# Kernel optimization log

Hardware: AMD Instinct MI355X
Metric: run time of the kernel (lower is better)

The kernel has to match this reference:

```python
import jax, jax.numpy as jnp
import numpy as np
from jax import lax

S = 0.5      # smoothing coefficient (constant in the layer)
EPS = 1e-6   # numerical floor (constant in the layer)


def setup_inputs() -> dict:
    key = jax.random.key(0)
    # [1, F, T] nonnegative spectrogram-like input
    data = jax.random.uniform(key, (1, 1024, 16384), dtype=jnp.float32)
    alpha = jnp.float32(0.98)
    r = jnp.float32(0.5)
    delta = jnp.float32(2.0)
    return {"data": data, "alpha": alpha, "r": r, "delta": delta}


def _ema_over_time(x):
    # x: [F, T]; first-order IIR: m_t = (1-s)*m_{t-1} + s*x_t, m_{-1} = 0
    def step(carry, xt):  # carry, xt: [F]
        m = (1.0 - S) * carry + S * xt
        return m, m
    _, M = lax.scan(step, jnp.zeros(x.shape[0], x.dtype), x.T)  # M: [T, F]
    return M.T  # [F, T]


def reference(data, alpha, r, delta):
    # Original layer computes the smoother M from batch element 0 only
    M = _ema_over_time(data[0])[None]          # [1, F, T]
    Mepow = (M + EPS) ** alpha                  # AGC gain
    pcen = (data / Mepow + delta) ** r - delta ** r
    return pcen
```

## Files before the change

### kernel.cpp

```cpp
#include <hip/hip_runtime.h>


static constexpr int F = 1024;
static constexpr int T = 16384;
static constexpr int C = 16;
static constexpr int BLOCK = 256;
static constexpr int HALF = BLOCK * C;
static constexpr int TPB = T / HALF;
static constexpr int SEEDQ = C / 4;
static constexpr int NQ = HALF / 4 + SEEDQ;
static constexpr int QPT = C / 4;
static constexpr float EPS = 1e-6f;

__device__ __forceinline__ int swz(int q) { return q ^ ((q >> 3) & 7); }

__device__ __forceinline__ void async_ld16(const float4* g, float4* l) {
  __builtin_amdgcn_global_load_lds(
      (const __attribute__((address_space(1))) void*)g,
      (__attribute__((address_space(3))) void*)l, 16, 0, 0);
}

__global__ __launch_bounds__(BLOCK) void pcen_kernel(
    const float* __restrict__ data,
    const float* __restrict__ alpha_p,
    const float* __restrict__ r_p,
    const float* __restrict__ delta_p,
    float* __restrict__ out)
{
  __shared__ float4 lds4[NQ];

  const int tid = threadIdx.x;
  const int bid = blockIdx.x;
  const int f = bid >> 2;
  const int h = bid & (TPB - 1);
  const size_t base = (size_t)f * T + (size_t)h * HALF;
  const float4* __restrict__ g4 = reinterpret_cast<const float4*>(data + base);
  float4* __restrict__ o4 = reinterpret_cast<float4*>(out + base);

  {
    const int wavebase = tid & ~63;
    #pragma unroll
    for (int i = 0; i < QPT; ++i) {
      const int p = SEEDQ + i * BLOCK + tid;
      async_ld16(g4 + (swz(p) - SEEDQ), &lds4[SEEDQ + i * BLOCK + wavebase]);
    }
    if (tid < SEEDQ) {
      if (h) {
        async_ld16(g4 - SEEDQ + tid, &lds4[0]);
      } else {
        lds4[tid] = make_float4(0.f, 0.f, 0.f, 0.f);
      }
    }
  }
  __syncthreads();

  const float alpha = alpha_p[0];
  const float r     = r_p[0];
  const float delta = delta_p[0];
  const bool  rhalf = (r == 0.5f);
  const float delta_r = rhalf ? sqrtf(delta) : exp2f(r * log2f(delta));

  const int tq = tid * QPT;

  float m = 0.0f;
  #pragma unroll
  for (int k = 0; k < QPT; ++k) {
    float4 v = lds4[swz(tq + k)];
    m = 0.5f * (m + v.x);
    m = 0.5f * (m + v.y);
    m = 0.5f * (m + v.z);
    m = 0.5f * (m + v.w);
  }

  float4 res[QPT];

  #define PCEN_ELEM(XX, OO, POW)                        \
    { m = 0.5f * (m + (XX));                            \
      float lgm = log2f(m + EPS);                       \
      float inv = exp2f(-alpha * lgm);    \
      float qq  = fmaf((XX), inv, delta);               \
      OO = (POW) - delta_r; }

  if (rhalf) {
    #pragma unroll
    for (int k = 0; k < QPT; ++k) {
      float4 v = lds4[swz(SEEDQ + tq + k)];
      float4 o;
      PCEN_ELEM(v.x, o.x, sqrtf(qq));
      PCEN_ELEM(v.y, o.y, sqrtf(qq));
      PCEN_ELEM(v.z, o.z, sqrtf(qq));
      PCEN_ELEM(v.w, o.w, sqrtf(qq));
      res[k] = o;
    }
  } else {
    #pragma unroll
    for (int k = 0; k < QPT; ++k) {
      float4 v = lds4[swz(SEEDQ + tq + k)];
      float4 o;
      PCEN_ELEM(v.x, o.x, exp2f(r * log2f(qq)));
      PCEN_ELEM(v.y, o.y, exp2f(r * log2f(qq)));
      PCEN_ELEM(v.z, o.z, exp2f(r * log2f(qq)));
      PCEN_ELEM(v.w, o.w, exp2f(r * log2f(qq)));
      res[k] = o;
    }
  }
  #undef PCEN_ELEM

  __syncthreads();

  #pragma unroll
  for (int k = 0; k < QPT; ++k) lds4[swz(SEEDQ + tq + k)] = res[k];

  __syncthreads();

  #pragma unroll
  for (int i = 0; i < QPT; ++i) {
    const int p = SEEDQ + i * BLOCK + tid;
    o4[p - SEEDQ] = lds4[swz(p)];
  }
}

extern "C" void kernel_launch(void* const* d_in, const int* in_sizes, int n_in,
                              void* d_out, int out_size, void* d_ws, size_t ws_size,
                              hipStream_t stream) {
  const float* data  = (const float*)d_in[0];
  const float* alpha = (const float*)d_in[1];
  const float* r     = (const float*)d_in[2];
  const float* delta = (const float*)d_in[3];
  float* out = (float*)d_out;

  const int grid = F * TPB;
  pcen_kernel<<<dim3(grid), dim3(BLOCK), 0, stream>>>(data, alpha, r, delta, out);
}
```

Before: 30.58 us.

## Load inputs directly from global per thread, drop LDS staging on the load path

Replaces the async global-to-LDS staging of inputs with direct per-thread float4 global loads of the thread's own 16-element chunk plus the preceding 16 elements used to seed the EMA. This removes one barrier and the LDS round-trip on input. It also swaps in native log2/exp2/sqrt intrinsics, adds an occupancy hint to launch bounds, and uses nontemporal stores for the output. The cost is that each input element is fetched twice from global memory (the seed reads overlap the neighbouring thread's chunk), and the per-thread strided loads are uncoalesced, 64 bytes apart across lanes.

```diff
diff --git a/kernel.cpp b/kernel.cpp
--- a/kernel.cpp
+++ b/kernel.cpp
@@ -5,118 +5,112 @@
 static constexpr int T = 16384;
 static constexpr int C = 16;
 static constexpr int BLOCK = 256;
-static constexpr int HALF = BLOCK * C;
-static constexpr int TPB = T / HALF;
-static constexpr int SEEDQ = C / 4;
-static constexpr int NQ = HALF / 4 + SEEDQ;
-static constexpr int QPT = C / 4;
+static constexpr int TILE = BLOCK * C;
+static constexpr int QT = TILE / 4;
 static constexpr float EPS = 1e-6f;
+
+typedef float v4f __attribute__((ext_vector_type(4)));
 
 __device__ __forceinline__ int swz(int q) { return q ^ ((q >> 3) & 7); }
 
-__device__ __forceinline__ void async_ld16(const float4* g, float4* l) {
-  __builtin_amdgcn_global_load_lds(
-      (const __attribute__((address_space(1))) void*)g,
-      (__attribute__((address_space(3))) void*)l, 16, 0, 0);
-}
+#if __has_builtin(__builtin_amdgcn_logf)
+__device__ __forceinline__ float nlog2(float x) { return __builtin_amdgcn_logf(x); }
+#else
+__device__ __forceinline__ float nlog2(float x) { return log2f(x); }
+#endif
+#if __has_builtin(__builtin_amdgcn_exp2f)
+__device__ __forceinline__ float nexp2(float x) { return __builtin_amdgcn_exp2f(x); }
+#else
+__device__ __forceinline__ float nexp2(float x) { return exp2f(x); }
+#endif
+#if __has_builtin(__builtin_amdgcn_sqrtf)
+__device__ __forceinline__ float nsqrt(float x) { return __builtin_amdgcn_sqrtf(x); }
+#else
+__device__ __forceinline__ float nsqrt(float x) { return sqrtf(x); }
+#endif
 
-__global__ __launch_bounds__(BLOCK) void pcen_kernel(
+__global__ __launch_bounds__(BLOCK, 8) void pcen_kernel(
     const float* __restrict__ data,
     const float* __restrict__ alpha_p,
     const float* __restrict__ r_p,
     const float* __restrict__ delta_p,
     float* __restrict__ out)
 {
-  __shared__ float4 lds4[NQ];
+  __shared__ v4f lds4[QT];
 
   const int tid = threadIdx.x;
   const int bid = blockIdx.x;
   const int f = bid >> 2;
-  const int h = bid & (TPB - 1);
-  const size_t base = (size_t)f * T + (size_t)h * HALF;
-  const float4* __restrict__ g4 = reinterpret_cast<const float4*>(data + base);
-  float4* __restrict__ o4 = reinterpret_cast<float4*>(out + base);
+  const int h = bid & 3;
+  const size_t tilebase = (size_t)f * T + (size_t)h * TILE;
+  const size_t tbase = tilebase + (size_t)tid * C;
 
-  {
-    const int wavebase = tid & ~63;
+  float m = 0.0f;
+  if ((h | tid) != 0) {
+    const v4f* __restrict__ xs =
+        reinterpret_cast<const v4f*>(data + tbase - C);
     #pragma unroll
-    for (int i = 0; i < QPT; ++i) {
-      const int p = SEEDQ + i * BLOCK + tid;
-      async_ld16(g4 + (swz(p) - SEEDQ), &lds4[SEEDQ + i * BLOCK + wavebase]);
-    }
-    if (tid < SEEDQ) {
-      if (h) {
-        async_ld16(g4 - SEEDQ + tid, &lds4[0]);
-      } else {
-        lds4[tid] = make_float4(0.f, 0.f, 0.f, 0.f);
-      }
+    for (int k = 0; k < 4; ++k) {
+      v4f v = xs[k];
+      m = 0.5f * (m + v.x);
+      m = 0.5f * (m + v.y);
+      m = 0.5f * (m + v.z);
+      m = 0.5f * (m + v.w);
     }
   }
-  __syncthreads();
 
   const float alpha = alpha_p[0];
   const float r     = r_p[0];
   const float delta = delta_p[0];
   const bool  rhalf = (r == 0.5f);
-  const float delta_r = rhalf ? sqrtf(delta) : exp2f(r * log2f(delta));
+  const float delta_r = rhalf ? nsqrt(delta) : nexp2(r * nlog2(delta));
 
-  const int tq = tid * QPT;
-
-  float m = 0.0f;
-  #pragma unroll
-  for (int k = 0; k < QPT; ++k) {
-    float4 v = lds4[swz(tq + k)];
-    m = 0.5f * (m + v.x);
-    m = 0.5f * (m + v.y);
-    m = 0.5f * (m + v.z);
-    m = 0.5f * (m + v.w);
-  }
-
-  float4 res[QPT];
+  const v4f* __restrict__ xm = reinterpret_cast<const v4f*>(data + tbase);
+  v4f res[4];
 
   #define PCEN_ELEM(XX, OO, POW)                        \
     { m = 0.5f * (m + (XX));                            \
-      float lgm = log2f(m + EPS);                       \
-      float inv = exp2f(-alpha * lgm);    \
+      float lgm = nlog2(m + EPS);                       \
+      float inv = nexp2(-alpha * lgm);    \
       float qq  = fmaf((XX), inv, delta);               \
       OO = (POW) - delta_r; }
 
   if (rhalf) {
     #pragma unroll
-    for (int k = 0; k < QPT; ++k) {
-      float4 v = lds4[swz(SEEDQ + tq + k)];
-      float4 o;
-      PCEN_ELEM(v.x, o.x, sqrtf(qq));
-      PCEN_ELEM(v.y, o.y, sqrtf(qq));
-      PCEN_ELEM(v.z, o.z, sqrtf(qq));
-      PCEN_ELEM(v.w, o.w, sqrtf(qq));
+    for (int k = 0; k < 4; ++k) {
+      v4f v = xm[k];
+      v4f o;
+      PCEN_ELEM(v.x, o.x, nsqrt(qq));
+      PCEN_ELEM(v.y, o.y, nsqrt(qq));
+      PCEN_ELEM(v.z, o.z, nsqrt(qq));
+      PCEN_ELEM(v.w, o.w, nsqrt(qq));
       res[k] = o;
     }
   } else {
     #pragma unroll
-    for (int k = 0; k < QPT; ++k) {
-      float4 v = lds4[swz(SEEDQ + tq + k)];
-      float4 o;
-      PCEN_ELEM(v.x, o.x, exp2f(r * log2f(qq)));
-      PCEN_ELEM(v.y, o.y, exp2f(r * log2f(qq)));
-      PCEN_ELEM(v.z, o.z, exp2f(r * log2f(qq)));
-      PCEN_ELEM(v.w, o.w, exp2f(r * log2f(qq)));
+    for (int k = 0; k < 4; ++k) {
+      v4f v = xm[k];
+      v4f o;
+      PCEN_ELEM(v.x, o.x, nexp2(r * nlog2(qq)));
+      PCEN_ELEM(v.y, o.y, nexp2(r * nlog2(qq)));
+      PCEN_ELEM(v.z, o.z, nexp2(r * nlog2(qq)));
+      PCEN_ELEM(v.w, o.w, nexp2(r * nlog2(qq)));
       res[k] = o;
     }
   }
   #undef PCEN_ELEM
 
-  __syncthreads();
-
+  const int tq = tid * 4;
   #pragma unroll
-  for (int k = 0; k < QPT; ++k) lds4[swz(SEEDQ + tq + k)] = res[k];
+  for (int k = 0; k < 4; ++k) lds4[swz(tq + k)] = res[k];
 
   __syncthreads();
 
+  v4f* __restrict__ o4 = reinterpret_cast<v4f*>(out + tilebase);
   #pragma unroll
-  for (int i = 0; i < QPT; ++i) {
-    const int p = SEEDQ + i * BLOCK + tid;
-    o4[p - SEEDQ] = lds4[swz(p)];
+  for (int i = 0; i < 4; ++i) {
+    const int p = i * BLOCK + tid;
+    __builtin_nontemporal_store(lds4[swz(p)], o4 + p);
   }
 }
 
@@ -129,6 +123,6 @@
   const float* delta = (const float*)d_in[3];
   float* out = (float*)d_out;
 
-  const int grid = F * TPB;
+  const int grid = F * (T / TILE);
   pcen_kernel<<<dim3(grid), dim3(BLOCK), 0, stream>>>(data, alpha, r, delta, out);
 }
```

Measured after the change: 25.61 us. 1.19x faster.
